# Performance work log

Hardware: AMD Instinct MI355X
Metric: run time of the kernel (lower is better)

Reference implementation:

```python
import jax, jax.numpy as jnp
import numpy as np

B, C1, C2, HEADS = 8, 256, 512, 8
HD = C1 // HEADS
H3, W3, H4, W4 = 128, 128, 64, 64
EPS = 1e-5

def _ln(x, g, b):
    m = jnp.mean(x, -1, keepdims=True)
    v = jnp.mean((x - m) ** 2, -1, keepdims=True)
    return (x - m) * jax.lax.rsqrt(v + EPS) * g + b

def _pool(x, k):
    b, c, h, w = x.shape
    return x.reshape(b, c, h // k, k, w // k, k).mean(axis=(3, 5))

def _resize(x, h, w):
    b, c = x.shape[:2]
    return jax.image.resize(x, (b, c, h, w), method='bilinear')

def setup_inputs():
    key = jax.random.key(0)
    ks = jax.random.split(key, 12)
    w = lambda k, s: jax.random.normal(k, s, jnp.float32) * 0.02
    z = lambda *s: jnp.zeros(s, jnp.float32)
    o = lambda *s: jnp.ones(s, jnp.float32)
    return {
        'a3': jax.random.normal(ks[0], (B, C1, H3, W3), jnp.float32),
        'a4': jax.random.normal(ks[1], (B, C2, H4, W4), jnp.float32),
        'conv_w': w(ks[2], (C1, C2)), 'conv_b': z(C1),
        'bn_g': o(C1), 'bn_b': z(C1), 'bn_rm': z(C1), 'bn_rv': o(C1),
        'wq': w(ks[3], (C1, C1)), 'bq': z(C1), 'lnq_g': o(C1), 'lnq_b': z(C1),
        'wk': w(ks[4], (C1, C1)), 'bk': z(C1), 'lnk_g': o(C1), 'lnk_b': z(C1),
        'wv': w(ks[5], (C1, C1)), 'bv': z(C1),
        'wo': w(ks[6], (C1, C1)), 'bo': z(C1),
        'w1': w(ks[7], (4 * C1, C1)), 'b1': z(4 * C1),
        'w2': w(ks[8], (C1, 4 * C1)), 'b2': z(C1),
        'n1_g': o(C1), 'n1_b': z(C1), 'n2_g': o(C1), 'n2_b': z(C1),
        'idx': 11,
    }

def _forward(a3, a4, conv_w, conv_b, bn_g, bn_b, bn_rm, bn_rv, wq, bq, lnq_g, lnq_b,
             wk, bk, lnk_g, lnk_b, wv, bv, wo, bo, w1, b1, w2, b2,
             n1_g, n1_b, n2_g, n2_b, idx):
    # 1x1 conv (high_to_low_embed) + eval-mode BatchNorm2d
    a4e = jnp.einsum('bchw,oc->bohw', a4, conv_w) + conv_b[:, None, None]
    a4e = (a4e - bn_rm[:, None, None]) * (bn_g * jax.lax.rsqrt(bn_rv + EPS))[:, None, None] + bn_b[:, None, None]
    if idx == 11:
        a3d = _pool(a3, 2)
    else:
        a3d = _pool(a3, 4)
        a4e = _pool(a4e, 2)
    b, c, h, w = a3d.shape
    H, W = a4e.shape[2:]
    a3f = a3d.reshape(b, c, h * w).transpose(0, 2, 1)   # [b, Nq, c1]
    a4f = a4e.reshape(b, c, H * W).transpose(0, 2, 1)   # [b, Nk, c1]
    Q = _ln(a3f @ wq.T + bq, lnq_g, lnq_b)
    K = _ln(a4f @ wk.T + bk, lnk_g, lnk_b)
    V = a4f @ wv.T + bv
    Q = jax.nn.relu(Q.reshape(b, h * w, HEADS, HD).transpose(0, 2, 3, 1))  # [b,h,d,Nq]
    K = jax.nn.relu(K.reshape(b, H * W, HEADS, HD).transpose(0, 2, 3, 1))  # [b,h,d,Nk]
    V = V.reshape(b, H * W, HEADS, HD).transpose(0, 2, 3, 1)               # [b,h,d,Nk]
    V = jnp.pad(V, ((0, 0), (0, 0), (0, 1), (0, 0)), constant_values=1.0)  # [b,h,d+1,Nk]
    VK = jnp.einsum('bhen,bhdn->bhed', V, K)            # [b,h,d+1,d]
    out = jnp.einsum('bhed,bhdq->bheq', VK, Q)          # [b,h,d+1,Nq]
    denom = jnp.maximum(out[:, :, -1:], EPS)            # clamp(min=eps)
    out = out[:, :, :-1] / denom                        # [b,h,d,Nq]
    # replicate torch: out.transpose(1,2).contiguous().view(bs,-1,heads*head_dim)
    out = jnp.swapaxes(out, 1, 2).reshape(b, h * w, HEADS * HD)
    out = out @ wo.T + bo
    # transformer FFN branch: computed by the original module but not in its returned outputs
    src = _ln(a3f + out, n1_g, n1_b)
    ffn = jax.nn.gelu(src @ w1.T + b1, approximate=False) @ w2.T + b2
    src = _ln(src + ffn, n2_g, n2_b)
    del src  # dead in original return as well
    a3_sa = out.transpose(0, 2, 1).reshape(b, c, h, w)
    a3_sa = _resize(a3_sa, a3.shape[2], a3.shape[3]) * a3
    a4_up = _resize(a4, a4.shape[2] * 2, a4.shape[3] * 2)
    return a3_sa, a4_up

def reference(a3, a4, conv_w, conv_b, bn_g, bn_b, bn_rm, bn_rv, wq, bq, lnq_g, lnq_b,
              wk, bk, lnk_g, lnk_b, wv, bv, wo, bo, w1, b1, w2, b2,
              n1_g, n1_b, n2_g, n2_b, idx):
    return _forward(a3, a4, conv_w, conv_b, bn_g, bn_b, bn_rm, bn_rv, wq, bq, lnq_g, lnq_b,
                    wk, bk, lnk_g, lnk_b, wv, bv, wo, bo, w1, b1, w2, b2,
                    n1_g, n1_b, n2_g, n2_b, idx)
```

## Files before the change

### kernel.cpp

```cpp
#include <hip/hip_runtime.h>
#include <cstdint>
#include <cstddef>

typedef unsigned short u16;
typedef __bf16 bf16x8 __attribute__((ext_vector_type(8)));
typedef float f32x4 __attribute__((ext_vector_type(4)));

#define EPS_ 1e-5f

__device__ __forceinline__ float bf2f(u16 u){
  union { uint32_t i; float f; } v; v.i = ((uint32_t)u) << 16; return v.f;
}
__device__ __forceinline__ u16 f2bf(float f){
  union { float f; uint32_t i; } v; v.f = f;
  uint32_t u = v.i;
  u += 0x7fffu + ((u >> 16) & 1u);
  return (u16)(u >> 16);
}
__device__ __forceinline__ void gload_lds16(const void* g, void* l){
  __builtin_amdgcn_global_load_lds((const __attribute__((address_space(1))) uint32_t*)g,
                                   (__attribute__((address_space(3))) uint32_t*)l, 16, 0, 0);
}

#define OFF_WKV   ((size_t)0)
#define OFF_WQB   ((size_t)524288)
#define OFF_WOB   ((size_t)655360)
#define OFF_BKV   ((size_t)786432)
#define OFF_A3DT  ((size_t)2097152)
#define OFF_Q     ((size_t)18874368)

#define OUT1_A4T  ((size_t)0)
#define OUT1_KV   ((size_t)33554432)
#define OUT1_ATT  ((size_t)67108864)
#define OUT1_PROJ ((size_t)83886080)
#define OUT1_VK   ((size_t)117440512)
#define OUT1_VKB  ((size_t)121765888)

__global__ __launch_bounds__(256) void k_fold(
    const float* __restrict__ conv_w, const float* __restrict__ conv_b,
    const float* __restrict__ bn_g, const float* __restrict__ bn_b,
    const float* __restrict__ bn_rm, const float* __restrict__ bn_rv,
    const float* __restrict__ wk, const float* __restrict__ bk,
    const float* __restrict__ wv, const float* __restrict__ bv,
    u16* __restrict__ WKV, float* __restrict__ bkv){
  int n = blockIdx.x;
  int t = threadIdx.x;
  const float* wrow = (n < 256) ? (wk + (size_t)n*256) : (wv + (size_t)(n-256)*256);
  __shared__ float sw[256], st_[256];
  {
    float s  = bn_g[t] * rsqrtf(bn_rv[t] + EPS_);
    float tt = s * (conv_b[t] - bn_rm[t]) + bn_b[t];
    float w = wrow[t];
    sw[t] = w * s;
    st_[t] = w * tt;
  }
  __syncthreads();
  for (int cc = 0; cc < 2; ++cc){
    int c = t + cc*256;
    float acc = 0.f;
    #pragma unroll 8
    for (int o = 0; o < 256; ++o)
      acc += sw[o] * conv_w[(size_t)o*512 + c];
    WKV[(size_t)n*512 + c] = f2bf(acc);
  }
  if (t == 0){
    float acc = (n < 256) ? bk[n] : bv[n-256];
    for (int o = 0; o < 256; ++o) acc += st_[o];
    bkv[n] = acc;
  }
}

__global__ __launch_bounds__(256) void k_cvt2(const float* __restrict__ wq, const float* __restrict__ wo,
                                              u16* __restrict__ WQB, u16* __restrict__ WOB){
  int bidx = blockIdx.x;
  const float* src = (bidx < 256) ? wq : wo;
  u16* dst = (bidx < 256) ? WQB : WOB;
  int i = (bidx & 255)*256 + threadIdx.x;
  dst[i] = f2bf(src[i]);
}

__global__ __launch_bounds__(256) void k_pool_a3(const float* __restrict__ a3, u16* __restrict__ a3dT){
  int y = blockIdx.x;
  int c0 = blockIdx.y * 32;
  int b = blockIdx.z;
  int t = threadIdx.x;
  __shared__ float ld[32*257];
  const float* src = a3 + (((size_t)(b*256 + c0))*128 + 2*y)*128;
  #pragma unroll
  for (int cc = 0; cc < 32; ++cc)
    ld[cc*257 + t] = src[(size_t)cc*16384 + t];
  __syncthreads();
  int cc = t & 31, xb = t >> 5;
  u16* dst = a3dT + ((size_t)b*4096 + y*64)*256 + c0 + cc;
  #pragma unroll
  for (int xi = 0; xi < 8; ++xi){
    int x = xb*8 + xi;
    const float* r = &ld[cc*257 + 2*x];
    float v = 0.25f*(r[0] + r[1] + r[128] + r[129]);
    dst[(size_t)x*256] = f2bf(v);
  }
}

__global__ __launch_bounds__(256) void k_tr_a4(const float* __restrict__ a4, u16* __restrict__ a4T){
  int y = blockIdx.x;
  int c0 = blockIdx.y * 32;
  int b = blockIdx.z;
  int t = threadIdx.x;
  __shared__ float ld[32*65];
  const float* src = a4 + (((size_t)(b*512 + c0))*64 + y)*64;
  #pragma unroll
  for (int i = 0; i < 8; ++i){
    int idx = i*256 + t;
    int cc = idx >> 6, x = idx & 63;
    ld[cc*65 + x] = src[(size_t)cc*4096 + x];
  }
  __syncthreads();
  int cc = t & 31, xb = t >> 5;
  u16* dst = a4T + ((size_t)b*4096 + y*64)*512 + c0 + cc;
  #pragma unroll
  for (int xi = 0; xi < 8; ++xi){
    int x = xb*8 + xi;
    dst[(size_t)x*512] = f2bf(ld[cc*65 + x]);
  }
}

template<int KDIM, int NDIM, int SMODE>
__global__ __launch_bounds__(256) void k_gemm(
    const u16* __restrict__ A, const u16* __restrict__ Bw,
    const float* __restrict__ bias, void* __restrict__ Cout){
  __shared__ alignas(16) u16 lA[128*32];
  __shared__ alignas(16) u16 lB[128*32];
  int m0 = blockIdx.x * 128, n0 = blockIdx.y * 128;
  int t = threadIdx.x;
  int lane = t & 63, wid = t >> 6;
  int wm = wid >> 1, wn = wid & 1;
  int fr = lane & 15, fq = lane >> 4;
  f32x4 acc[4][4] = {};
  const u16* Abase = A + (size_t)m0 * KDIM;
  const u16* Bbase = Bw + (size_t)n0 * KDIM;
  for (int kt = 0; kt < KDIM/32; ++kt){
    #pragma unroll
    for (int i = 0; i < 2; ++i){
      int u = i*256 + t;
      gload_lds16(Abase + (size_t)(u>>2)*KDIM + kt*32 + (u&3)*8, lA + u*8);
      gload_lds16(Bbase + (size_t)(u>>2)*KDIM + kt*32 + (u&3)*8, lB + u*8);
    }
    __syncthreads();
    bf16x8 af[4], bfr[4];
    #pragma unroll
    for (int fm = 0; fm < 4; ++fm)
      af[fm] = *(const bf16x8*)&lA[(wm*64 + fm*16 + fr)*32 + fq*8];
    #pragma unroll
    for (int fn = 0; fn < 4; ++fn)
      bfr[fn] = *(const bf16x8*)&lB[(wn*64 + fn*16 + fr)*32 + fq*8];
    #pragma unroll
    for (int fm = 0; fm < 4; ++fm)
      #pragma unroll
      for (int fn = 0; fn < 4; ++fn)
        acc[fm][fn] = __builtin_amdgcn_mfma_f32_16x16x32_bf16(af[fm], bfr[fn], acc[fm][fn], 0, 0, 0);
    __syncthreads();
  }
  #pragma unroll
  for (int fn = 0; fn < 4; ++fn){
    int j = n0 + wn*64 + fn*16 + fr;
    float bj = bias[j];
    #pragma unroll
    for (int fm = 0; fm < 4; ++fm){
      int m = m0 + wm*64 + fm*16 + fq*4;
      if constexpr (SMODE == 0){
        u16* C = (u16*)Cout;
        #pragma unroll
        for (int i = 0; i < 4; ++i)
          C[(size_t)(m + i)*NDIM + j] = f2bf(acc[fm][fn][i] + bj);
      } else {
        int b = m >> 12, p = m & 4095;
        size_t base = ((size_t)(b*NDIM + j))*4096 + p;
        u16* C = (u16*)Cout;
        ushort4 pk;
        pk.x = f2bf(acc[fm][fn][0] + bj);
        pk.y = f2bf(acc[fm][fn][1] + bj);
        pk.z = f2bf(acc[fm][fn][2] + bj);
        pk.w = f2bf(acc[fm][fn][3] + bj);
        *(ushort4*)&C[base] = pk;
      }
    }
  }
}

__global__ __launch_bounds__(256) void k_ln_row(u16* __restrict__ X,
    const float* __restrict__ g, const float* __restrict__ bb){
  int row = blockIdx.x*4 + (threadIdx.x >> 6);
  int lane = threadIdx.x & 63;
  u16* p = X + (size_t)row*256 + lane*4;
  ushort4 v4 = *(const ushort4*)p;
  float v0 = bf2f(v4.x), v1 = bf2f(v4.y), v2 = bf2f(v4.z), v3 = bf2f(v4.w);
  float s = v0+v1+v2+v3;
  float s2 = v0*v0+v1*v1+v2*v2+v3*v3;
  #pragma unroll
  for (int off = 32; off > 0; off >>= 1){
    s  += __shfl_down(s, off);
    s2 += __shfl_down(s2, off);
  }
  s = __shfl(s, 0); s2 = __shfl(s2, 0);
  float mean = s * (1.f/256.f);
  float var = s2 * (1.f/256.f) - mean*mean;
  float r = rsqrtf(var + EPS_);
  float4 gg = *(const float4*)&g[lane*4];
  float4 b4 = *(const float4*)&bb[lane*4];
  ushort4 o;
  o.x = f2bf(fmaxf((v0-mean)*r*gg.x + b4.x, 0.f));
  o.y = f2bf(fmaxf((v1-mean)*r*gg.y + b4.y, 0.f));
  o.z = f2bf(fmaxf((v2-mean)*r*gg.z + b4.z, 0.f));
  o.w = f2bf(fmaxf((v3-mean)*r*gg.w + b4.w, 0.f));
  *(ushort4*)p = o;
}

__global__ __launch_bounds__(256) void k_ln_col(u16* __restrict__ KV,
    const float* __restrict__ g, const float* __restrict__ bb){
  int p0 = blockIdx.x * 128;
  int b = blockIdx.y;
  int t = threadIdx.x;
  __shared__ uint32_t lds32[256*66];
  __shared__ float sA[256], sB[256];
  __shared__ float meanA[128], rstdA[128];
  u16* tile = (u16*)lds32;
  int c = t & 63;
  int w = t >> 6;
  #pragma unroll 8
  for (int i = 0; i < 64; ++i){
    int j = i*4 + w;
    uint32_t v = ((const uint32_t*)(KV + ((size_t)(b*512 + j))*4096 + p0))[c];
    lds32[j*66 + c] = v;
  }
  __syncthreads();
  {
    int p = t & 127, jh = t >> 7;
    float s = 0.f, s2 = 0.f;
    #pragma unroll 8
    for (int jj = 0; jj < 128; ++jj){
      float v = bf2f(tile[(jh*128 + jj)*132 + p]);
      s += v; s2 += v*v;
    }
    sA[t] = s; sB[t] = s2;
  }
  __syncthreads();
  if (t < 128){
    float st = sA[t] + sA[128 + t];
    float s2t = sB[t] + sB[128 + t];
    float mean = st * (1.f/256.f);
    float var = s2t * (1.f/256.f) - mean*mean;
    meanA[t] = mean;
    rstdA[t] = rsqrtf(var + EPS_);
  }
  __syncthreads();
  float m0v = meanA[2*c], m1v = meanA[2*c + 1];
  float r0 = rstdA[2*c], r1 = rstdA[2*c + 1];
  #pragma unroll 8
  for (int i = 0; i < 64; ++i){
    int j = i*4 + w;
    uint32_t v = lds32[j*66 + c];
    float v0 = bf2f((u16)(v & 0xffffu));
    float v1 = bf2f((u16)(v >> 16));
    float gj = g[j], bj = bb[j];
    u16 o0 = f2bf(fmaxf((v0 - m0v)*r0*gj + bj, 0.f));
    u16 o1 = f2bf(fmaxf((v1 - m1v)*r1*gj + bj, 0.f));
    ((uint32_t*)(KV + ((size_t)(b*512 + j))*4096 + p0))[c] = (uint32_t)o0 | ((uint32_t)o1 << 16);
  }
}

__global__ __launch_bounds__(64) void k_vk(const u16* __restrict__ KV, float* __restrict__ VKp){
  int chunk = blockIdx.x;
  int bh = blockIdx.y;
  int b = bh >> 3, h = bh & 7;
  int lane = threadIdx.x;
  __shared__ alignas(16) u16 lK[32*256];
  __shared__ alignas(16) u16 lV[32*256];
  int n0 = chunk * 256;
  const u16* Ks = KV + ((size_t)(b*512 + h*32))*4096 + n0;
  const u16* Vs = KV + ((size_t)(b*512 + 256 + h*32))*4096 + n0;
  #pragma unroll
  for (int i = 0; i < 16; ++i){
    int u = i*64 + lane;
    int row = u >> 5, cb = (u & 31)*8;
    gload_lds16(Ks + (size_t)row*4096 + cb, lK + u*8);
    gload_lds16(Vs + (size_t)row*4096 + cb, lV + u*8);
  }
  __builtin_amdgcn_s_waitcnt(0);
  __syncthreads();
  int fr = lane & 15, fq = lane >> 4;
  f32x4 acc[2][2] = {};
  #pragma unroll
  for (int ks = 0; ks < 8; ++ks){
    bf16x8 av0 = *(const bf16x8*)&lV[(fr)*256 + ks*32 + fq*8];
    bf16x8 av1 = *(const bf16x8*)&lV[(16+fr)*256 + ks*32 + fq*8];
    bf16x8 bk0 = *(const bf16x8*)&lK[(fr)*256 + ks*32 + fq*8];
    bf16x8 bk1 = *(const bf16x8*)&lK[(16+fr)*256 + ks*32 + fq*8];
    acc[0][0] = __builtin_amdgcn_mfma_f32_16x16x32_bf16(av0, bk0, acc[0][0], 0,0,0);
    acc[0][1] = __builtin_amdgcn_mfma_f32_16x16x32_bf16(av0, bk1, acc[0][1], 0,0,0);
    acc[1][0] = __builtin_amdgcn_mfma_f32_16x16x32_bf16(av1, bk0, acc[1][0], 0,0,0);
    acc[1][1] = __builtin_amdgcn_mfma_f32_16x16x32_bf16(av1, bk1, acc[1][1], 0,0,0);
  }
  float* dst = VKp + ((size_t)bh*16 + chunk)*(33*32);
  #pragma unroll
  for (int fe = 0; fe < 2; ++fe)
    #pragma unroll
    for (int fd = 0; fd < 2; ++fd)
      #pragma unroll
      for (int i = 0; i < 4; ++i){
        int e = fe*16 + fq*4 + i;
        int d = fd*16 + fr;
        dst[e*32 + d] = acc[fe][fd][i];
      }
  {
    int d = lane & 31, half = lane >> 5;
    float s = 0.f;
    #pragma unroll
    for (int i = 0; i < 16; ++i){
      bf16x8 kv = *(const bf16x8*)&lK[d*256 + half*128 + i*8];
      #pragma unroll
      for (int j = 0; j < 8; ++j) s += (float)kv[j];
    }
    s += __shfl_down(s, 32);
    if (lane < 32) dst[32*32 + d] = s;
  }
}

__global__ __launch_bounds__(256) void k_cvt_vk(const float* __restrict__ VKp, u16* __restrict__ VKb){
  int i = blockIdx.x*256 + threadIdx.x;
  int bh = i / (48*32);
  int r = i - bh*48*32;
  int e = r >> 5, d = r & 31;
  float v = 0.f;
  if (e < 33){
    const float* p = VKp + (size_t)bh*16*(33*32) + e*32 + d;
    #pragma unroll
    for (int c = 0; c < 16; ++c) v += p[(size_t)c*(33*32)];
  }
  VKb[i] = f2bf(v);
}

__global__ __launch_bounds__(256) void k_att(const u16* __restrict__ Q,
    const u16* __restrict__ VKb, u16* __restrict__ ATT){
  int qc = blockIdx.x;
  int bh = blockIdx.y;
  int b = bh >> 3, h = bh & 7;
  int t = threadIdx.x;
  int lane = t & 63, wid = t >> 6;
  int fr = lane & 15, fq = lane >> 4;
  int q0 = qc*256 + wid*64;
  const u16* Qb = Q + ((size_t)(b*4096 + q0))*256 + h*32 + fq*8;
  bf16x8 aq[4];
  #pragma unroll
  for (int fm = 0; fm < 4; ++fm)
    aq[fm] = *(const bf16x8*)&Qb[(size_t)(fm*16 + fr)*256];
  const u16* Vb = VKb + (size_t)bh*48*32;
  bf16x8 bv_[3];
  #pragma unroll
  for (int fn = 0; fn < 3; ++fn)
    bv_[fn] = *(const bf16x8*)&Vb[(fn*16 + fr)*32 + fq*8];
  f32x4 acc[4][3] = {};
  #pragma unroll
  for (int fm = 0; fm < 4; ++fm)
    #pragma unroll
    for (int fn = 0; fn < 3; ++fn)
      acc[fm][fn] = __builtin_amdgcn_mfma_f32_16x16x32_bf16(aq[fm], bv_[fn], acc[fm][fn], 0,0,0);
  __shared__ alignas(16) u16 latt[32*264];
  #pragma unroll
  for (int fm = 0; fm < 4; ++fm){
    #pragma unroll
    for (int i = 0; i < 4; ++i){
      float dv = __shfl(acc[fm][2][i], lane & 48);
      float rd = 1.0f / fmaxf(dv, EPS_);
      int qloc = wid*64 + fm*16 + fq*4 + i;
      latt[(fr)*264 + qloc]      = f2bf(acc[fm][0][i] * rd);
      latt[(16 + fr)*264 + qloc] = f2bf(acc[fm][1][i] * rd);
    }
  }
  __syncthreads();
  int row = t >> 3, seg = t & 7;
  u16* dst = ATT + ((size_t)(b*4096 + row*128 + h*16 + qc))*256 + seg*32;
  const u16* srcl = &latt[row*264 + seg*32];
  #pragma unroll
  for (int k = 0; k < 4; ++k)
    *(uint4*)&dst[k*8] = *(const uint4*)&srcl[k*8];
}

__device__ __forceinline__ void bil_idx(int o, int n, int &i0, int &i1, float &w0, float &w1){
  float s = 0.5f*(float)o - 0.25f;
  float fl = floorf(s);
  i0 = (int)fl; i1 = i0 + 1;
  w1 = s - fl; w0 = 1.f - w1;
  if (i0 < 0){ i0 = 0; w0 = 0.f; w1 = 1.f; }
  if (i1 > n-1){ i1 = n-1; w1 = 0.f; w0 = 1.f; }
}

__global__ __launch_bounds__(256) void k_resize_mul_a3(const u16* __restrict__ PROJ,
    const float* __restrict__ a3, float* __restrict__ out0){
  int bc = blockIdx.x;
  int t = threadIdx.x;
  __shared__ float P[4096];
  const uint32_t* src = (const uint32_t*)(PROJ + (size_t)bc*4096);
  #pragma unroll
  for (int i = 0; i < 8; ++i){
    uint32_t v = src[i*256 + t];
    P[(i*256 + t)*2]     = bf2f((u16)(v & 0xffffu));
    P[(i*256 + t)*2 + 1] = bf2f((u16)(v >> 16));
  }
  __syncthreads();
  const float* ap = a3 + (size_t)bc*16384;
  float* op = out0 + (size_t)bc*16384;
  for (int k = 0; k < 64; ++k){
    int px = k*256 + t;
    int Y = px >> 7, X = px & 127;
    int y0,y1,x0,x1; float wy0,wy1,wx0,wx1;
    bil_idx(Y, 64, y0,y1,wy0,wy1);
    bil_idx(X, 64, x0,x1,wx0,wx1);
    float v = wy0*(wx0*P[y0*64+x0] + wx1*P[y0*64+x1])
            + wy1*(wx0*P[y1*64+x0] + wx1*P[y1*64+x1]);
    op[px] = v * ap[px];
  }
}

__global__ __launch_bounds__(256) void k_resize_a4(const float* __restrict__ a4, float* __restrict__ out1){
  int bc = blockIdx.x;
  int t = threadIdx.x;
  __shared__ float P[4096];
  const float* src = a4 + (size_t)bc*4096;
  #pragma unroll
  for (int i = 0; i < 16; ++i) P[i*256 + t] = src[i*256 + t];
  __syncthreads();
  float* op = out1 + (size_t)bc*16384;
  for (int k = 0; k < 64; ++k){
    int px = k*256 + t;
    int Y = px >> 7, X = px & 127;
    int y0,y1,x0,x1; float wy0,wy1,wx0,wx1;
    bil_idx(Y, 64, y0,y1,wy0,wy1);
    bil_idx(X, 64, x0,x1,wx0,wx1);
    op[px] = wy0*(wx0*P[y0*64+x0] + wx1*P[y0*64+x1])
           + wy1*(wx0*P[y1*64+x0] + wx1*P[y1*64+x1]);
  }
}

extern "C" void kernel_launch(void* const* d_in, const int* in_sizes, int n_in,
                              void* d_out, int out_size, void* d_ws, size_t ws_size,
                              hipStream_t stream){
  (void)in_sizes; (void)n_in; (void)out_size; (void)ws_size;
  const float* a3     = (const float*)d_in[0];
  const float* a4     = (const float*)d_in[1];
  const float* conv_w = (const float*)d_in[2];
  const float* conv_b = (const float*)d_in[3];
  const float* bn_g   = (const float*)d_in[4];
  const float* bn_b   = (const float*)d_in[5];
  const float* bn_rm  = (const float*)d_in[6];
  const float* bn_rv  = (const float*)d_in[7];
  const float* wq     = (const float*)d_in[8];
  const float* bq     = (const float*)d_in[9];
  const float* lnq_g  = (const float*)d_in[10];
  const float* lnq_b  = (const float*)d_in[11];
  const float* wk     = (const float*)d_in[12];
  const float* bk     = (const float*)d_in[13];
  const float* lnk_g  = (const float*)d_in[14];
  const float* lnk_b  = (const float*)d_in[15];
  const float* wv     = (const float*)d_in[16];
  const float* bv     = (const float*)d_in[17];
  const float* wo     = (const float*)d_in[18];
  const float* bo     = (const float*)d_in[19];

  float* out0 = (float*)d_out;
  float* out1 = out0 + (size_t)33554432;

  char* ws = (char*)d_ws;
  u16*   WKV  = (u16*)(ws + OFF_WKV);
  u16*   WQB  = (u16*)(ws + OFF_WQB);
  u16*   WOB  = (u16*)(ws + OFF_WOB);
  float* BKV  = (float*)(ws + OFF_BKV);
  u16*   A3DT = (u16*)(ws + OFF_A3DT);
  u16*   Qw   = (u16*)(ws + OFF_Q);

  char* o1 = (char*)out1;
  u16*   A4T  = (u16*)(o1 + OUT1_A4T);
  u16*   KVw  = (u16*)(o1 + OUT1_KV);
  u16*   ATT  = (u16*)(o1 + OUT1_ATT);
  u16*   PROJ = (u16*)(o1 + OUT1_PROJ);
  float* VKp  = (float*)(o1 + OUT1_VK);
  u16*   VKB  = (u16*)(o1 + OUT1_VKB);

  k_fold<<<512, 256, 0, stream>>>(conv_w, conv_b, bn_g, bn_b, bn_rm, bn_rv,
                                  wk, bk, wv, bv, WKV, BKV);
  k_cvt2<<<512, 256, 0, stream>>>(wq, wo, WQB, WOB);

  k_pool_a3<<<dim3(64, 8, 8), 256, 0, stream>>>(a3, A3DT);
  k_tr_a4<<<dim3(64, 16, 8), 256, 0, stream>>>(a4, A4T);

  k_gemm<256, 256, 0><<<dim3(256, 2), 256, 0, stream>>>(A3DT, WQB, bq, (void*)Qw);
  k_gemm<512, 512, 1><<<dim3(256, 4), 256, 0, stream>>>(A4T, WKV, BKV, (void*)KVw);

  k_ln_row<<<8192, 256, 0, stream>>>(Qw, lnq_g, lnq_b);
  k_ln_col<<<dim3(32, 8), 256, 0, stream>>>(KVw, lnk_g, lnk_b);

  k_vk<<<dim3(16, 64), 64, 0, stream>>>(KVw, VKp);
  k_cvt_vk<<<384, 256, 0, stream>>>(VKp, VKB);
  k_att<<<dim3(16, 64), 256, 0, stream>>>(Qw, VKB, ATT);

  k_gemm<256, 256, 1><<<dim3(256, 2), 256, 0, stream>>>(ATT, WOB, bo, (void*)PROJ);

  k_resize_mul_a3<<<2048, 256, 0, stream>>>(PROJ, a3, out0);
  k_resize_a4<<<4096, 256, 0, stream>>>(a4, out1);
}
```

Measured before the change: 785.5 us.

## Fuse K layernorm with V·K reduction and merge weight conversion into fold

The column layernorm on K is merged with the per-chunk V·Kᵀ MFMA accumulation, so the normalized K stays in LDS instead of being written back to global memory and reloaded. The K loads are widened to 16-byte vectors, and the gamma/beta values are staged in LDS. The wq/wo bf16 conversion is folded into the k_fold launch as extra blocks, which removes one kernel launch. In exchange the partial-sum buffer doubles to 32 chunks per head, the final reduction grows to match, and V fragments are now read directly from global memory.

```diff
diff --git a/kernel.cpp b/kernel.cpp
--- a/kernel.cpp
+++ b/kernel.cpp
@@ -34,7 +34,7 @@
 #define OUT1_ATT  ((size_t)67108864)
 #define OUT1_PROJ ((size_t)83886080)
 #define OUT1_VK   ((size_t)117440512)
-#define OUT1_VKB  ((size_t)121765888)
+#define OUT1_VKB  ((size_t)126091264)
 
 __global__ __launch_bounds__(256) void k_fold(
     const float* __restrict__ conv_w, const float* __restrict__ conv_b,
@@ -42,9 +42,18 @@
     const float* __restrict__ bn_rm, const float* __restrict__ bn_rv,
     const float* __restrict__ wk, const float* __restrict__ bk,
     const float* __restrict__ wv, const float* __restrict__ bv,
-    u16* __restrict__ WKV, float* __restrict__ bkv){
+    const float* __restrict__ wq, const float* __restrict__ wo,
+    u16* __restrict__ WKV, float* __restrict__ bkv,
+    u16* __restrict__ WQB, u16* __restrict__ WOB){
   int n = blockIdx.x;
   int t = threadIdx.x;
+  if (n >= 512){
+    const float* src = (n < 768) ? wq : wo;
+    u16* dst = (n < 768) ? WQB : WOB;
+    int i = (n & 255)*256 + t;
+    dst[i] = f2bf(src[i]);
+    return;
+  }
   const float* wrow = (n < 256) ? (wk + (size_t)n*256) : (wv + (size_t)(n-256)*256);
   __shared__ float sw[256], st_[256];
   {
@@ -68,15 +77,6 @@
     for (int o = 0; o < 256; ++o) acc += st_[o];
     bkv[n] = acc;
   }
-}
-
-__global__ __launch_bounds__(256) void k_cvt2(const float* __restrict__ wq, const float* __restrict__ wo,
-                                              u16* __restrict__ WQB, u16* __restrict__ WOB){
-  int bidx = blockIdx.x;
-  const float* src = (bidx < 256) ? wq : wo;
-  u16* dst = (bidx < 256) ? WQB : WOB;
-  int i = (bidx & 255)*256 + threadIdx.x;
-  dst[i] = f2bf(src[i]);
 }
 
 __global__ __launch_bounds__(256) void k_pool_a3(const float* __restrict__ a3, u16* __restrict__ a3dT){
@@ -215,22 +215,25 @@
   *(ushort4*)p = o;
 }
 
-__global__ __launch_bounds__(256) void k_ln_col(u16* __restrict__ KV,
-    const float* __restrict__ g, const float* __restrict__ bb){
-  int p0 = blockIdx.x * 128;
+__global__ __launch_bounds__(256) void k_lnvk(const u16* __restrict__ KV,
+    const float* __restrict__ g, const float* __restrict__ bb, float* __restrict__ VKp){
+  int pc = blockIdx.x;
+  int p0 = pc * 128;
   int b = blockIdx.y;
   int t = threadIdx.x;
-  __shared__ uint32_t lds32[256*66];
+  __shared__ uint32_t lds32[256*68];
   __shared__ float sA[256], sB[256];
   __shared__ float meanA[128], rstdA[128];
+  __shared__ float sG[256], sBb[256];
   u16* tile = (u16*)lds32;
-  int c = t & 63;
-  int w = t >> 6;
-  #pragma unroll 8
-  for (int i = 0; i < 64; ++i){
-    int j = i*4 + w;
-    uint32_t v = ((const uint32_t*)(KV + ((size_t)(b*512 + j))*4096 + p0))[c];
-    lds32[j*66 + c] = v;
+  sG[t] = g[t]; sBb[t] = bb[t];
+  int rg = t >> 4;
+  int l16 = t & 15;
+  #pragma unroll 4
+  for (int i = 0; i < 16; ++i){
+    int j = i*16 + rg;
+    uint4 v = *(const uint4*)(KV + ((size_t)(b*512 + j))*4096 + p0 + l16*8);
+    *(uint4*)&lds32[j*68 + l16*4] = v;
   }
   __syncthreads();
   {
@@ -238,7 +241,7 @@
     float s = 0.f, s2 = 0.f;
     #pragma unroll 8
     for (int jj = 0; jj < 128; ++jj){
-      float v = bf2f(tile[(jh*128 + jj)*132 + p]);
+      float v = bf2f(tile[(jh*128 + jj)*136 + p]);
       s += v; s2 += v*v;
     }
     sA[t] = s; sB[t] = s2;
@@ -253,75 +256,71 @@
     rstdA[t] = rsqrtf(var + EPS_);
   }
   __syncthreads();
-  float m0v = meanA[2*c], m1v = meanA[2*c + 1];
-  float r0 = rstdA[2*c], r1 = rstdA[2*c + 1];
-  #pragma unroll 8
-  for (int i = 0; i < 64; ++i){
-    int j = i*4 + w;
-    uint32_t v = lds32[j*66 + c];
-    float v0 = bf2f((u16)(v & 0xffffu));
-    float v1 = bf2f((u16)(v >> 16));
-    float gj = g[j], bj = bb[j];
-    u16 o0 = f2bf(fmaxf((v0 - m0v)*r0*gj + bj, 0.f));
-    u16 o1 = f2bf(fmaxf((v1 - m1v)*r1*gj + bj, 0.f));
-    ((uint32_t*)(KV + ((size_t)(b*512 + j))*4096 + p0))[c] = (uint32_t)o0 | ((uint32_t)o1 << 16);
-  }
-}
-
-__global__ __launch_bounds__(64) void k_vk(const u16* __restrict__ KV, float* __restrict__ VKp){
-  int chunk = blockIdx.x;
-  int bh = blockIdx.y;
-  int b = bh >> 3, h = bh & 7;
-  int lane = threadIdx.x;
-  __shared__ alignas(16) u16 lK[32*256];
-  __shared__ alignas(16) u16 lV[32*256];
-  int n0 = chunk * 256;
-  const u16* Ks = KV + ((size_t)(b*512 + h*32))*4096 + n0;
-  const u16* Vs = KV + ((size_t)(b*512 + 256 + h*32))*4096 + n0;
-  #pragma unroll
+  float mm[8], rr[8];
+  #pragma unroll
+  for (int k = 0; k < 8; ++k){
+    mm[k] = meanA[l16*8 + k];
+    rr[k] = rstdA[l16*8 + k];
+  }
+  #pragma unroll 4
   for (int i = 0; i < 16; ++i){
-    int u = i*64 + lane;
-    int row = u >> 5, cb = (u & 31)*8;
-    gload_lds16(Ks + (size_t)row*4096 + cb, lK + u*8);
-    gload_lds16(Vs + (size_t)row*4096 + cb, lV + u*8);
-  }
-  __builtin_amdgcn_s_waitcnt(0);
-  __syncthreads();
+    int j = i*16 + rg;
+    uint32_t* rowp = &lds32[j*68 + l16*4];
+    uint4 v = *(uint4*)rowp;
+    float gj = sG[j], bj = sBb[j];
+    uint32_t w_[4] = {v.x, v.y, v.z, v.w};
+    #pragma unroll
+    for (int w2 = 0; w2 < 4; ++w2){
+      float v0 = bf2f((u16)(w_[w2] & 0xffffu));
+      float v1 = bf2f((u16)(w_[w2] >> 16));
+      u16 o0 = f2bf(fmaxf((v0 - mm[2*w2])*rr[2*w2]*gj + bj, 0.f));
+      u16 o1 = f2bf(fmaxf((v1 - mm[2*w2+1])*rr[2*w2+1]*gj + bj, 0.f));
+      w_[w2] = (uint32_t)o0 | ((uint32_t)o1 << 16);
+    }
+    uint4 ov; ov.x = w_[0]; ov.y = w_[1]; ov.z = w_[2]; ov.w = w_[3];
+    *(uint4*)rowp = ov;
+  }
+  __syncthreads();
+  int lane = t & 63, wid = t >> 6;
   int fr = lane & 15, fq = lane >> 4;
-  f32x4 acc[2][2] = {};
-  #pragma unroll
-  for (int ks = 0; ks < 8; ++ks){
-    bf16x8 av0 = *(const bf16x8*)&lV[(fr)*256 + ks*32 + fq*8];
-    bf16x8 av1 = *(const bf16x8*)&lV[(16+fr)*256 + ks*32 + fq*8];
-    bf16x8 bk0 = *(const bf16x8*)&lK[(fr)*256 + ks*32 + fq*8];
-    bf16x8 bk1 = *(const bf16x8*)&lK[(16+fr)*256 + ks*32 + fq*8];
-    acc[0][0] = __builtin_amdgcn_mfma_f32_16x16x32_bf16(av0, bk0, acc[0][0], 0,0,0);
-    acc[0][1] = __builtin_amdgcn_mfma_f32_16x16x32_bf16(av0, bk1, acc[0][1], 0,0,0);
-    acc[1][0] = __builtin_amdgcn_mfma_f32_16x16x32_bf16(av1, bk0, acc[1][0], 0,0,0);
-    acc[1][1] = __builtin_amdgcn_mfma_f32_16x16x32_bf16(av1, bk1, acc[1][1], 0,0,0);
-  }
-  float* dst = VKp + ((size_t)bh*16 + chunk)*(33*32);
-  #pragma unroll
-  for (int fe = 0; fe < 2; ++fe)
-    #pragma unroll
-    for (int fd = 0; fd < 2; ++fd)
+  #pragma unroll
+  for (int hh = 0; hh < 2; ++hh){
+    int h = wid*2 + hh;
+    f32x4 acc[2][2] = {};
+    #pragma unroll
+    for (int ks = 0; ks < 4; ++ks){
+      bf16x8 kf0 = *(const bf16x8*)&tile[(h*32 + fr)*136 + ks*32 + fq*8];
+      bf16x8 kf1 = *(const bf16x8*)&tile[(h*32 + 16 + fr)*136 + ks*32 + fq*8];
+      const u16* Vb = KV + ((size_t)(b*512 + 256 + h*32 + fr))*4096 + p0 + ks*32 + fq*8;
+      bf16x8 vf0 = *(const bf16x8*)Vb;
+      bf16x8 vf1 = *(const bf16x8*)(Vb + (size_t)16*4096);
+      acc[0][0] = __builtin_amdgcn_mfma_f32_16x16x32_bf16(vf0, kf0, acc[0][0], 0,0,0);
+      acc[0][1] = __builtin_amdgcn_mfma_f32_16x16x32_bf16(vf0, kf1, acc[0][1], 0,0,0);
+      acc[1][0] = __builtin_amdgcn_mfma_f32_16x16x32_bf16(vf1, kf0, acc[1][0], 0,0,0);
+      acc[1][1] = __builtin_amdgcn_mfma_f32_16x16x32_bf16(vf1, kf1, acc[1][1], 0,0,0);
+    }
+    float* dst = VKp + (((size_t)(b*8 + h))*32 + pc)*1056;
+    #pragma unroll
+    for (int et = 0; et < 2; ++et)
       #pragma unroll
-      for (int i = 0; i < 4; ++i){
-        int e = fe*16 + fq*4 + i;
-        int d = fd*16 + fr;
-        dst[e*32 + d] = acc[fe][fd][i];
-      }
+      for (int dt = 0; dt < 2; ++dt)
+        #pragma unroll
+        for (int i = 0; i < 4; ++i){
+          int e = et*16 + fq*4 + i;
+          int d = dt*16 + fr;
+          dst[e*32 + d] = acc[et][dt][i];
+        }
+  }
   {
-    int d = lane & 31, half = lane >> 5;
+    int h = t >> 5, d = t & 31;
+    int j = h*32 + d;
     float s = 0.f;
-    #pragma unroll
-    for (int i = 0; i < 16; ++i){
-      bf16x8 kv = *(const bf16x8*)&lK[d*256 + half*128 + i*8];
-      #pragma unroll
-      for (int j = 0; j < 8; ++j) s += (float)kv[j];
-    }
-    s += __shfl_down(s, 32);
-    if (lane < 32) dst[32*32 + d] = s;
+    #pragma unroll 8
+    for (int i = 0; i < 64; ++i){
+      uint32_t x = lds32[j*68 + i];
+      s += bf2f((u16)(x & 0xffffu)) + bf2f((u16)(x >> 16));
+    }
+    VKp[(((size_t)(b*8 + h))*32 + pc)*1056 + 32*32 + d] = s;
   }
 }
 
@@ -332,9 +331,9 @@
   int e = r >> 5, d = r & 31;
   float v = 0.f;
   if (e < 33){
-    const float* p = VKp + (size_t)bh*16*(33*32) + e*32 + d;
-    #pragma unroll
-    for (int c = 0; c < 16; ++c) v += p[(size_t)c*(33*32)];
+    const float* p = VKp + (size_t)bh*32*1056 + e*32 + d;
+    #pragma unroll
+    for (int c = 0; c < 32; ++c) v += p[(size_t)c*1056];
   }
   VKb[i] = f2bf(v);
 }
@@ -485,9 +484,8 @@
   float* VKp  = (float*)(o1 + OUT1_VK);
   u16*   VKB  = (u16*)(o1 + OUT1_VKB);
 
-  k_fold<<<512, 256, 0, stream>>>(conv_w, conv_b, bn_g, bn_b, bn_rm, bn_rv,
-                                  wk, bk, wv, bv, WKV, BKV);
-  k_cvt2<<<512, 256, 0, stream>>>(wq, wo, WQB, WOB);
+  k_fold<<<1024, 256, 0, stream>>>(conv_w, conv_b, bn_g, bn_b, bn_rm, bn_rv,
+                                   wk, bk, wv, bv, wq, wo, WKV, BKV, WQB, WOB);
 
   k_pool_a3<<<dim3(64, 8, 8), 256, 0, stream>>>(a3, A3DT);
   k_tr_a4<<<dim3(64, 16, 8), 256, 0, stream>>>(a4, A4T);
@@ -496,9 +494,8 @@
   k_gemm<512, 512, 1><<<dim3(256, 4), 256, 0, stream>>>(A4T, WKV, BKV, (void*)KVw);
 
   k_ln_row<<<8192, 256, 0, stream>>>(Qw, lnq_g, lnq_b);
-  k_ln_col<<<dim3(32, 8), 256, 0, stream>>>(KVw, lnk_g, lnk_b);
-
-  k_vk<<<dim3(16, 64), 64, 0, stream>>>(KVw, VKp);
+
+  k_lnvk<<<dim3(32, 8), 256, 0, stream>>>(KVw, lnk_g, lnk_b, VKp);
   k_cvt_vk<<<384, 256, 0, stream>>>(VKp, VKB);
   k_att<<<dim3(16, 64), 256, 0, stream>>>(Qw, VKB, ATT);
 
```

Result: no change. 774.9 us (-1.4%).
